# Performance work log

Measured on AMD Instinct MI355X. Metric: run time of the kernel, lower is better.

The kernel has to match this reference:

```python
import jax, jax.numpy as jnp
import numpy as np

DIM = 1024
HEADS = 8
HD = DIM // HEADS          # 128
HALF = HD // 2             # 64 complex pairs
EPS = 1e-6
T, L, H, W = 10, 4, 21, 37
TOK_PER_FRAME = 1 + L * (5 + H * W)   # 3129
SK = T * TOK_PER_FRAME                # 31290
SQ = 512
THETA = 10000.0


def _inv_freqs(dim):
    # matches precompute_freqs_cis: 1/theta**(arange(0,dim,2)/dim)
    return 1.0 / THETA ** (np.arange(0, dim, 2)[: dim // 2].astype(np.float64) / dim)


def _angles(t_idx, h_idx, w_idx):
    # 3D RoPE split per precompute_freqs_cis_3d: f gets HD-2*(HD//3)=44 dims, h/w get HD//3=42 each
    hd3 = HD // 3
    inv_f = _inv_freqs(HD - 2 * hd3)  # 22 freqs
    inv_h = _inv_freqs(hd3)           # 21 freqs
    inv_w = _inv_freqs(hd3)           # 21 freqs
    ang = np.concatenate([
        t_idx[:, None] * inv_f[None, :],
        h_idx[:, None] * inv_h[None, :],
        w_idx[:, None] * inv_w[None, :],
    ], axis=-1)  # [S, 64]
    return ang


def _memory_positions():
    # per-frame layout from build_3d_freqs_unified: 1 pose token (h=w=0),
    # then per layer: 5 register tokens (h=w=0) + H*W grid tokens
    h_f, w_f = [0], [0]
    grid_h, grid_w = np.meshgrid(np.arange(H), np.arange(W), indexing='ij')
    for _ in range(L):
        h_f += [0] * 5 + list(grid_h.ravel())
        w_f += [0] * 5 + list(grid_w.ravel())
    h_f = np.asarray(h_f, np.float64)
    w_f = np.asarray(w_f, np.float64)
    t_idx = np.repeat(np.arange(T, dtype=np.float64), TOK_PER_FRAME)
    return t_idx, np.tile(h_f, T), np.tile(w_f, T)


def setup_inputs() -> dict:
    key = jax.random.key(0)
    ks = jax.random.split(key, 8)
    # RoPE angle tables
    tq = np.zeros(SQ)  # use_time_encoding=False for queries -> t=0
    hq = (np.arange(SQ) // W) % H
    wq = np.arange(SQ) % W
    ang_q = _angles(tq.astype(np.float64), hq.astype(np.float64), wq.astype(np.float64))
    tk, hk, wk = _memory_positions()
    ang_k = _angles(tk, hk, wk)
    s = 0.02
    inp = {
        'x': jax.random.normal(ks[0], (1, SQ, DIM), jnp.float32),
        'mem': jax.random.normal(ks[1], (1, SK, DIM), jnp.float32),
        'mask': jax.random.randint(ks[2], (1, SK), 0, 2) > 0,
        'cos_q': jnp.asarray(np.cos(ang_q), jnp.float32),
        'sin_q': jnp.asarray(np.sin(ang_q), jnp.float32),
        'cos_k': jnp.asarray(np.cos(ang_k), jnp.float32),
        'sin_k': jnp.asarray(np.sin(ang_k), jnp.float32),
        'Wq': jax.random.normal(ks[3], (DIM, DIM), jnp.float32) * s,
        'bq': jnp.zeros((DIM,), jnp.float32),
        'Wk': jax.random.normal(ks[4], (DIM, DIM), jnp.float32) * s,
        'bk': jnp.zeros((DIM,), jnp.float32),
        'Wv': jax.random.normal(ks[5], (DIM, DIM), jnp.float32) * s,
        'bv': jnp.zeros((DIM,), jnp.float32),
        'Wo': jax.random.normal(ks[6], (DIM, DIM), jnp.float32) * s,
        'bo': jnp.zeros((DIM,), jnp.float32),
        'gq': jnp.ones((DIM,), jnp.float32),
        'gk': jnp.ones((DIM,), jnp.float32),
    }
    return inp


def _rmsnorm(x, g):
    xf = x.astype(jnp.float32)
    y = xf * jax.lax.rsqrt(jnp.mean(xf * xf, axis=-1, keepdims=True) + EPS)
    return y.astype(x.dtype) * g


def _rope(x, cos, sin):
    # x: [B,S,D]; complex rotation on interleaved pairs per head, freqs shared across heads
    B, S, _ = x.shape
    xh = x.reshape(B, S, HEADS, HALF, 2)
    xr, xi = xh[..., 0], xh[..., 1]
    c = cos[None, :, None, :]
    s = sin[None, :, None, :]
    orr = xr * c - xi * s
    oi = xr * s + xi * c
    return jnp.stack([orr, oi], axis=-1).reshape(B, S, HEADS * HD)


def reference(x, mem, mask, cos_q, sin_q, cos_k, sin_k,
              Wq, bq, Wk, bk, Wv, bv, Wo, bo, gq, gk):
    q = _rmsnorm(x @ Wq.T + bq, gq)
    k = _rmsnorm(mem @ Wk.T + bk, gk)
    v = mem @ Wv.T + bv
    q = _rope(q, cos_q, sin_q)
    k = _rope(k, cos_k, sin_k)
    B, Sq, _ = q.shape
    Sk = k.shape[1]
    qh = q.reshape(B, Sq, HEADS, HD)
    kh = k.reshape(B, Sk, HEADS, HD)
    vh = v.reshape(B, Sk, HEADS, HD)
    scores = jnp.einsum('bqnd,bknd->bnqk', qh, kh) / jnp.sqrt(jnp.float32(HD))
    bias = jnp.where(mask[:, None, None, :], 0.0, -jnp.inf).astype(scores.dtype)
    attn = jax.nn.softmax(scores + bias, axis=-1)
    out = jnp.einsum('bnqk,bknd->bqnd', attn, vh).reshape(B, Sq, DIM)
    return out @ Wo.T + bo
```

## Files before the change

### kernel.cpp

```cpp
#include <hip/hip_runtime.h>
#include <cstdint>

typedef __bf16 bf16;
typedef __bf16 bf16x8 __attribute__((ext_vector_type(8)));
typedef __bf16 bf16x4 __attribute__((ext_vector_type(4)));
typedef float f32x4 __attribute__((ext_vector_type(4)));

#define DEVINL __device__ __forceinline__

namespace {
constexpr int DIM = 1024, HEADS = 8, HD = 128, HALF = 64;
constexpr int SQ = 512;
constexpr int SK = 31290;
constexpr int SKP = 31488;
constexpr int NSPLIT = 24;
constexpr int NCHUNK = 31;

constexpr long OFF_MEMB = 0;
constexpr long OFF_XB   = OFF_MEMB + (long)SKP * DIM * 2;
constexpr long OFF_WKV  = OFF_XB + (long)SQ * DIM * 2;
constexpr long OFF_WQ   = OFF_WKV + 2048L * DIM * 2;
constexpr long OFF_WO   = OFF_WQ + (long)DIM * DIM * 2;
constexpr long OFF_BKV  = OFF_WO + (long)DIM * DIM * 2;
constexpr long OFF_KPRE = OFF_BKV + 2048L * 4;
constexpr long OFF_VT   = OFF_KPRE + (long)SKP * DIM * 2;
constexpr long OFF_QPRE = OFF_VT + (long)DIM * SKP * 2;
constexpr long OFF_QR   = OFF_QPRE + (long)SQ * DIM * 4;
constexpr long OFF_ML   = OFF_QR + (long)SQ * DIM * 2;
constexpr long OFF_AO   = OFF_ML + (long)NSPLIT * HEADS * SQ * 2 * 4;
constexpr long OFF_IDX  = OFF_AO + (long)SQ * DIM * 2;
constexpr long OFF_NKC  = OFF_IDX + 31744L * 4;
constexpr long OFF_CSM  = OFF_NKC + 64;
constexpr long OFF_CBS  = OFF_CSM + 256;
constexpr long OFF_OP   = OFF_MEMB;
}

DEVINL void gl_lds16(const void* g, void* l) {
  __builtin_amdgcn_global_load_lds(
      (__attribute__((address_space(1))) void*)(void*)g,
      (__attribute__((address_space(3))) void*)l, 16, 0, 0);
}


__global__ __launch_bounds__(1024) void k_scan1(const int* __restrict__ mask,
                                                int* __restrict__ csum) {
  int tid = threadIdx.x, lane = tid & 63, wv = tid >> 6;
  __shared__ int wsum[16];
  long i = (long)blockIdx.x * 1024 + tid;
  int m = (i < SK) ? (mask[i] != 0) : 0;
  unsigned long long bal = __ballot(m);
  if (lane == 0) wsum[wv] = (int)__popcll(bal);
  __syncthreads();
  if (tid == 0) {
    int tot = 0;
    #pragma unroll
    for (int j = 0; j < 16; ++j) tot += wsum[j];
    csum[blockIdx.x] = tot;
  }
}

__global__ __launch_bounds__(64) void k_scan2(const int* __restrict__ csum,
                                              int* __restrict__ cbase,
                                              int* __restrict__ nkcp) {
  int lane = threadIdx.x;
  int v = (lane < NCHUNK) ? csum[lane] : 0;
  int p = v;
  #pragma unroll
  for (int off = 1; off < 64; off <<= 1) {
    int t = __shfl_up(p, off);
    if (lane >= off) p += t;
  }
  if (lane < NCHUNK) cbase[lane] = p - v;
  if (lane == NCHUNK - 1) *nkcp = p;
}

__global__ __launch_bounds__(1024) void k_scan3(const int* __restrict__ mask,
                                                const int* __restrict__ cbase,
                                                int* __restrict__ idx) {
  int tid = threadIdx.x, lane = tid & 63, wv = tid >> 6;
  __shared__ int wsum[16];
  long i = (long)blockIdx.x * 1024 + tid;
  int m = (i < SK) ? (mask[i] != 0) : 0;
  unsigned long long bal = __ballot(m);
  int wpre = (int)__popcll(bal & ((1ull << lane) - 1ull));
  if (lane == 0) wsum[wv] = (int)__popcll(bal);
  __syncthreads();
  int woff = 0;
  #pragma unroll
  for (int j = 0; j < 16; ++j) woff += (j < wv) ? wsum[j] : 0;
  if (m) idx[cbase[blockIdx.x] + woff + wpre] = (int)i;
}


__global__ __launch_bounds__(256) void k_cvt_mem(const float* __restrict__ mem,
                                                 const int* __restrict__ idx,
                                                 const int* __restrict__ nkcp,
                                                 bf16* __restrict__ memb) {
  long i = (long)blockIdx.x * 256 + threadIdx.x;
  long e = i * 8;
  if (e >= (long)SKP * DIM) return;
  int row = (int)(e >> 10);
  int nkc = *nkcp;
  int lim = ((((nkc + 63) & ~63) + 255) & ~255);
  if (row >= lim) return;
  bf16x8 o;
  if (row < nkc) {
    long se = ((long)idx[row] << 10) + (e & 1023);
    float4 a = *(const float4*)(mem + se);
    float4 b = *(const float4*)(mem + se + 4);
    o[0] = (bf16)a.x; o[1] = (bf16)a.y; o[2] = (bf16)a.z; o[3] = (bf16)a.w;
    o[4] = (bf16)b.x; o[5] = (bf16)b.y; o[6] = (bf16)b.z; o[7] = (bf16)b.w;
  } else {
    #pragma unroll
    for (int j = 0; j < 8; ++j) o[j] = (bf16)0.0f;
  }
  *(bf16x8*)(memb + e) = o;
}

__global__ __launch_bounds__(256) void k_prep(const float* __restrict__ x,
    const float* __restrict__ Wq, const float* __restrict__ Wo,
    const float* __restrict__ Wk, const float* __restrict__ Wv,
    const float* __restrict__ bk, const float* __restrict__ bv,
    bf16* __restrict__ xb, bf16* __restrict__ WqB, bf16* __restrict__ WoB,
    bf16* __restrict__ WkvB, float* __restrict__ bKV) {
  long i = (long)blockIdx.x * 256 + threadIdx.x;
  constexpr long n_x = 65536, n_w = 131072;
  const float* src;
  bf16* dst;
  long off;
  if (i < n_x) { src = x; dst = xb; off = i; }
  else if (i < n_x + n_w) { src = Wq; dst = WqB; off = i - n_x; }
  else if (i < n_x + 2 * n_w) { src = Wo; dst = WoB; off = i - n_x - n_w; }
  else if (i < n_x + 2 * n_w + 262144) {
    long j = i - n_x - 2 * n_w;
    long e = j * 8;
    int n = (int)(e >> 10);
    const float* s2 = (n < 1024) ? (Wk + e) : (Wv + e - 1024L * 1024);
    float4 a = *(const float4*)(s2);
    float4 b = *(const float4*)(s2 + 4);
    bf16x8 o;
    o[0] = (bf16)a.x; o[1] = (bf16)a.y; o[2] = (bf16)a.z; o[3] = (bf16)a.w;
    o[4] = (bf16)b.x; o[5] = (bf16)b.y; o[6] = (bf16)b.z; o[7] = (bf16)b.w;
    *(bf16x8*)(WkvB + e) = o;
    if (j < 2048) bKV[j] = (j < 1024) ? bk[j] : bv[j - 1024];
    return;
  } else return;
  long e = off * 8;
  float4 a = *(const float4*)(src + e);
  float4 b = *(const float4*)(src + e + 4);
  bf16x8 o;
  o[0] = (bf16)a.x; o[1] = (bf16)a.y; o[2] = (bf16)a.z; o[3] = (bf16)a.w;
  o[4] = (bf16)b.x; o[5] = (bf16)b.y; o[6] = (bf16)b.z; o[7] = (bf16)b.w;
  *(bf16x8*)(dst + e) = o;
}


template<int MODE>
__global__ __launch_bounds__(256, 2)
void k_gemm(const bf16* __restrict__ A, const bf16* __restrict__ B,
            const float* __restrict__ bias, int Mtiles, int Ntiles,
            float* __restrict__ outF, int ldF,
            bf16* __restrict__ outK, bf16* __restrict__ outVT) {
  constexpr int K = 1024;
  __shared__ char lds[32768];
  char* ldsA = lds;
  char* ldsB = lds + 16384;
  int tid = threadIdx.x;
  int w = tid >> 6, lane = tid & 63;
  int cpx = gridDim.x >> 3;
  int bid = (blockIdx.x & 7) * cpx + (blockIdx.x >> 3);
  int mt = bid / Ntiles, nt = bid % Ntiles;
  int m0 = mt * 128, n0 = nt * 128;
  int wm = w >> 1, wn = w & 1;
  int cl = lane & 15, rg = lane >> 4;

  f32x4 acc[4][4] = {};

  int rowi = lane >> 3, g = lane & 7;
  for (int kt = 0; kt < K / 64; ++kt) {
    #pragma unroll
    for (int j = 0; j < 4; ++j) {
      int rb = (w * 4 + j) * 8;
      int row = rb + rowi;
      int gs = g ^ (row & 7);
      gl_lds16((const char*)(A + (long)(m0 + row) * K + kt * 64) + gs * 16, ldsA + rb * 128);
      gl_lds16((const char*)(B + (long)(n0 + row) * K + kt * 64) + gs * 16, ldsB + rb * 128);
    }
    __syncthreads();
    #pragma unroll
    for (int ks = 0; ks < 2; ++ks) {
      bf16x8 af[4], bfr[4];
      #pragma unroll
      for (int i = 0; i < 4; ++i) {
        int rowA = wm * 64 + i * 16 + cl;
        int c = ks * 4 + rg;
        af[i] = *(const bf16x8*)(ldsA + rowA * 128 + ((c ^ (rowA & 7)) * 16));
        int rowB = wn * 64 + i * 16 + cl;
        bfr[i] = *(const bf16x8*)(ldsB + rowB * 128 + ((c ^ (rowB & 7)) * 16));
      }
      #pragma unroll
      for (int mf = 0; mf < 4; ++mf)
        #pragma unroll
        for (int nf = 0; nf < 4; ++nf)
          acc[mf][nf] = __builtin_amdgcn_mfma_f32_16x16x32_bf16(af[mf], bfr[nf], acc[mf][nf], 0, 0, 0);
    }
    __syncthreads();
  }

  #pragma unroll
  for (int mf = 0; mf < 4; ++mf) {
    #pragma unroll
    for (int nf = 0; nf < 4; ++nf) {
      int n = n0 + wn * 64 + nf * 16 + cl;
      float bval = bias[n];
      int mb = m0 + wm * 64 + mf * 16 + rg * 4;
      #pragma unroll
      for (int rr = 0; rr < 4; ++rr)
        outF[(long)(mb + rr) * ldF + n] = acc[mf][nf][rr] + bval;
    }
  }
}


#define KV_PHASE(P)                                                                   \
  {                                                                                   \
    bf16x8 a00 = dsA(cur, 2 * (P), 0),     a01 = dsA(cur, 2 * (P), 1);                \
    bf16x8 a10 = dsA(cur, 2 * (P) + 1, 0), a11 = dsA(cur, 2 * (P) + 1, 1);            \
    __builtin_amdgcn_s_setprio(1);                                                    \
    _Pragma("unroll")                                                                 \
    for (int nf = 0; nf < 4; ++nf) {                                                  \
      acc[2 * (P)][nf]     = __builtin_amdgcn_mfma_f32_16x16x32_bf16(a00, bb[nf][0], acc[2 * (P)][nf], 0, 0, 0);     \
      acc[2 * (P) + 1][nf] = __builtin_amdgcn_mfma_f32_16x16x32_bf16(a10, bb[nf][0], acc[2 * (P) + 1][nf], 0, 0, 0); \
    }                                                                                 \
    _Pragma("unroll")                                                                 \
    for (int nf = 0; nf < 4; ++nf) {                                                  \
      acc[2 * (P)][nf]     = __builtin_amdgcn_mfma_f32_16x16x32_bf16(a01, bb[nf][1], acc[2 * (P)][nf], 0, 0, 0);     \
      acc[2 * (P) + 1][nf] = __builtin_amdgcn_mfma_f32_16x16x32_bf16(a11, bb[nf][1], acc[2 * (P) + 1][nf], 0, 0, 0); \
    }                                                                                 \
    __builtin_amdgcn_s_setprio(0);                                                    \
  }

__global__ __launch_bounds__(512)
void k_gemm_kv(const bf16* __restrict__ A, const bf16* __restrict__ B,
               const float* __restrict__ bias, const int* __restrict__ nkcp,
               bf16* __restrict__ outK, bf16* __restrict__ outVT) {
  constexpr int K = 1024, NTK = 16;
  __shared__ char lds[131072];
  const int tid = threadIdx.x;
  const int w = tid >> 6, lane = tid & 63;
  const int mt = blockIdx.x >> 3, nt = blockIdx.x & 7;
  const int m0 = mt * 256, n0 = nt * 256;
  if (m0 >= ((*nkcp + 63) & ~63)) return;
  const int wm = w >> 2, wn = w & 3;
  const int cl = lane & 15, rg = lane >> 4;
  const int srow = lane >> 3, sg = lane & 7;

  f32x4 acc[8][4] = {};

  auto stage = [&](int b, int kt, int isB, int cr) {
    const bf16* src = isB ? B : A;
    int r = cr + w * 8 + srow;
    int gs = sg ^ (r & 7);
    const char* gp = (const char*)(src + (long)((isB ? n0 : m0) + r) * K + kt * 64) + gs * 16;
    char* lp = lds + b * 65536 + isB * 32768 + (cr + w * 8) * 128;
    gl_lds16(gp, lp);
  };
  auto dsA = [&](int b, int mf, int ks) -> bf16x8 {
    int r = wm * 128 + mf * 16 + cl;
    int c = ks * 4 + rg;
    return *(const bf16x8*)(lds + b * 65536 + r * 128 + ((c ^ (r & 7)) * 16));
  };
  auto dsB = [&](int b, int nf, int ks) -> bf16x8 {
    int r = wn * 64 + nf * 16 + cl;
    int c = ks * 4 + rg;
    return *(const bf16x8*)(lds + b * 65536 + 32768 + r * 128 + ((c ^ (r & 7)) * 16));
  };

  stage(0, 0, 1, 0);   stage(0, 0, 1, 64);
  stage(0, 0, 1, 128); stage(0, 0, 1, 192);
  stage(0, 0, 0, 0);   stage(0, 0, 0, 128);
  stage(0, 0, 0, 64);  stage(0, 0, 0, 192);

  for (int t = 0; t < NTK; ++t) {
    const int cur = t & 1, nxt = cur ^ 1;
    const bool pre = (t + 1 < NTK);
    bf16x8 bb[4][2];

    if (pre) {
      stage(nxt, t + 1, 1, 0); stage(nxt, t + 1, 1, 64);
      asm volatile("s_waitcnt vmcnt(4)\ns_barrier" ::: "memory");
    } else {
      asm volatile("s_waitcnt vmcnt(2)\ns_barrier" ::: "memory");
    }
    #pragma unroll
    for (int nf = 0; nf < 4; ++nf) { bb[nf][0] = dsB(cur, nf, 0); bb[nf][1] = dsB(cur, nf, 1); }
    KV_PHASE(0)
    asm volatile("s_barrier" ::: "memory");
    if (pre) {
      stage(nxt, t + 1, 1, 128); stage(nxt, t + 1, 1, 192);
      stage(nxt, t + 1, 0, 0);   stage(nxt, t + 1, 0, 128);
    }
    KV_PHASE(1)
    asm volatile("s_barrier" ::: "memory");
    if (pre) {
      stage(nxt, t + 1, 0, 64); stage(nxt, t + 1, 0, 192);
      asm volatile("s_waitcnt vmcnt(8)\ns_barrier" ::: "memory");
    } else {
      asm volatile("s_waitcnt vmcnt(0)\ns_barrier" ::: "memory");
    }
    KV_PHASE(2)
    asm volatile("s_barrier" ::: "memory");
    KV_PHASE(3)
    asm volatile("s_barrier" ::: "memory");
  }

  if (nt < 4) {
    #pragma unroll
    for (int mf = 0; mf < 8; ++mf)
      #pragma unroll
      for (int nf = 0; nf < 4; ++nf) {
        int n = n0 + wn * 64 + nf * 16 + cl;
        float bval = bias[n];
        int mrow = m0 + wm * 128 + mf * 16 + rg * 4;
        #pragma unroll
        for (int rr = 0; rr < 4; ++rr)
          outK[(long)(mrow + rr) * 1024 + n] = (bf16)(acc[mf][nf][rr] + bval);
      }
  } else {
    #pragma unroll
    for (int mf = 0; mf < 8; ++mf)
      #pragma unroll
      for (int nf = 0; nf < 4; ++nf) {
        int n = n0 + wn * 64 + nf * 16 + cl;
        float bval = bias[n];
        int mrow = m0 + wm * 128 + mf * 16 + rg * 4;
        bf16x4 pk;
        #pragma unroll
        for (int rr = 0; rr < 4; ++rr) pk[rr] = (bf16)(acc[mf][nf][rr] + bval);
        *(bf16x4*)(outVT + (long)(n - 1024) * SKP + mrow) = pk;
      }
  }
}


__global__ __launch_bounds__(256) void k_fuse_q(const float* __restrict__ QP,
    bf16* __restrict__ Qr, const float* __restrict__ gg,
    const float* __restrict__ cosT, const float* __restrict__ sinT) {
  int row = blockIdx.x, tid = threadIdx.x;
  int d0 = tid * 4;
  float4 t = *(const float4*)(QP + (long)row * DIM + d0);
  float v0 = t.x, v1 = t.y, v2 = t.z, v3 = t.w;
  float ss = v0 * v0 + v1 * v1 + v2 * v2 + v3 * v3;
  #pragma unroll
  for (int m = 1; m < 64; m <<= 1) ss += __shfl_xor(ss, m);
  __shared__ float red[4];
  if ((tid & 63) == 0) red[tid >> 6] = ss;
  __syncthreads();
  float rn = rsqrtf((red[0] + red[1] + red[2] + red[3]) * (1.0f / DIM) + 1e-6f);
  v0 *= rn * gg[d0]; v1 *= rn * gg[d0 + 1]; v2 *= rn * gg[d0 + 2]; v3 *= rn * gg[d0 + 3];
  int i0 = (d0 & 127) >> 1;
  float c0 = cosT[(long)row * HALF + i0], s0 = sinT[(long)row * HALF + i0];
  float c1 = cosT[(long)row * HALF + i0 + 1], s1 = sinT[(long)row * HALF + i0 + 1];
  bf16x4 o = { (bf16)(v0 * c0 - v1 * s0), (bf16)(v0 * s0 + v1 * c0),
               (bf16)(v2 * c1 - v3 * s1), (bf16)(v2 * s1 + v3 * c1) };
  *(bf16x4*)(Qr + (long)row * DIM + d0) = o;
}

__global__ __launch_bounds__(256) void k_fuse_k(bf16* __restrict__ KP,
    const float* __restrict__ gg, const float* __restrict__ cosT,
    const float* __restrict__ sinT, const int* __restrict__ idx,
    const int* __restrict__ nkcp) {
  int row = blockIdx.x, tid = threadIdx.x;
  int nkc = *nkcp;
  if (row >= ((nkc + 63) & ~63)) return;
  int orig = (row < nkc) ? idx[row] : 0;
  int d0 = tid * 4;
  bf16x4 t = *(const bf16x4*)(KP + (long)row * DIM + d0);
  float v0 = (float)t[0], v1 = (float)t[1], v2 = (float)t[2], v3 = (float)t[3];
  float ss = v0 * v0 + v1 * v1 + v2 * v2 + v3 * v3;
  #pragma unroll
  for (int m = 1; m < 64; m <<= 1) ss += __shfl_xor(ss, m);
  __shared__ float red[4];
  if ((tid & 63) == 0) red[tid >> 6] = ss;
  __syncthreads();
  float rn = rsqrtf((red[0] + red[1] + red[2] + red[3]) * (1.0f / DIM) + 1e-6f);
  v0 *= rn * gg[d0]; v1 *= rn * gg[d0 + 1]; v2 *= rn * gg[d0 + 2]; v3 *= rn * gg[d0 + 3];
  int i0 = (d0 & 127) >> 1;
  float c0 = cosT[(long)orig * HALF + i0], s0 = sinT[(long)orig * HALF + i0];
  float c1 = cosT[(long)orig * HALF + i0 + 1], s1 = sinT[(long)orig * HALF + i0 + 1];
  bf16x4 o = { (bf16)(v0 * c0 - v1 * s0), (bf16)(v0 * s0 + v1 * c0),
               (bf16)(v2 * c1 - v3 * s1), (bf16)(v2 * s1 + v3 * c1) };
  *(bf16x4*)(KP + (long)row * DIM + d0) = o;
}


__global__ __launch_bounds__(256, 2)
void k_attn(const bf16* __restrict__ Kr, const bf16* __restrict__ VT,
            const bf16* __restrict__ Qr, const int* __restrict__ nkcp,
            float* __restrict__ Opart, float* __restrict__ ml) {
  __shared__ char lds[51200];
  char* ldsK = lds;
  char* ldsV = lds + 16384;
  int tid = threadIdx.x, w = tid >> 6, lane = tid & 63;
  char* ldsP = lds + 32768 + w * 4608;
  int bid = blockIdx.x;
  int swz = (bid & 7) * 96 + (bid >> 3);
  int sp = swz >> 5, h = (swz >> 2) & 7, qb = swz & 3;
  int nkc = *nkcp;
  int NTC = (nkc + 63) >> 6;
  int t0 = (sp * NTC) / NSPLIT;
  int t1 = ((sp + 1) * NTC) / NSPLIT;
  int cl = lane & 15, rg = lane >> 4;
  int qbase = qb * 128 + w * 32;

  bf16x8 qf[2][4];
  #pragma unroll
  for (int mf = 0; mf < 2; ++mf)
    #pragma unroll
    for (int ks = 0; ks < 4; ++ks)
      qf[mf][ks] = *(const bf16x8*)(Qr + (long)(qbase + mf * 16 + cl) * DIM + h * HD + ks * 32 + rg * 8);

  f32x4 Oa[2][8] = {};
  float m_r[2] = {-1e30f, -1e30f};
  float l_r[2] = {0.f, 0.f};

  const float sc = 0.08838834764831845f;
  for (int t = t0; t < t1; ++t) {
    int k0 = t * 64;
    __syncthreads();
    {
      int rK = lane >> 4, gK = lane & 15;
      #pragma unroll
      for (int j = 0; j < 4; ++j) {
        int rb = w * 16 + j * 4;
        int row = rb + rK;
        int gs = gK ^ (row & 7);
        gl_lds16((const char*)(Kr + (long)(k0 + row) * DIM + h * HD) + gs * 16,
                 ldsK + rb * 256);
      }
      int rV = lane >> 3, gV = lane & 7;
      #pragma unroll
      for (int j = 0; j < 4; ++j) {
        int db = w * 32 + j * 8;
        int d = db + rV;
        int gs = gV ^ (d & 7);
        gl_lds16((const char*)(VT + (long)(h * HD + d) * SKP + k0) + gs * 16,
                 ldsV + db * 128);
      }
    }
    __syncthreads();

    f32x4 sa[2][4] = {};
    #pragma unroll
    for (int ks = 0; ks < 4; ++ks) {
      #pragma unroll
      for (int nf = 0; nf < 4; ++nf) {
        int key = nf * 16 + cl;
        int c = ks * 4 + rg;
        bf16x8 kb = *(const bf16x8*)(ldsK + key * 256 + ((c ^ (key & 7)) * 16));
        sa[0][nf] = __builtin_amdgcn_mfma_f32_16x16x32_bf16(kb, qf[0][ks], sa[0][nf], 0, 0, 0);
        sa[1][nf] = __builtin_amdgcn_mfma_f32_16x16x32_bf16(kb, qf[1][ks], sa[1][nf], 0, 0, 0);
      }
    }

    #pragma unroll
    for (int mf = 0; mf < 2; ++mf) {
      #pragma unroll
      for (int nf = 0; nf < 4; ++nf)
        #pragma unroll
        for (int r = 0; r < 4; ++r) {
          int key = k0 + nf * 16 + rg * 4 + r;
          sa[mf][nf][r] = (key < nkc) ? sa[mf][nf][r] * sc : -1e30f;
        }
      float mx = sa[mf][0][0];
      #pragma unroll
      for (int nf = 0; nf < 4; ++nf)
        #pragma unroll
        for (int r = 0; r < 4; ++r) mx = fmaxf(mx, sa[mf][nf][r]);
      mx = fmaxf(mx, __shfl_xor(mx, 16));
      mx = fmaxf(mx, __shfl_xor(mx, 32));
      bool grew = mx > m_r[mf] + 6.0f;
      if (__any(grew)) {
        float mn = grew ? mx : m_r[mf];
        float scl = __expf(m_r[mf] - mn);
        m_r[mf] = mn;
        l_r[mf] *= scl;
        int sb = lane & 48;
        float s0 = __shfl(scl, sb | (rg * 4 + 0));
        float s1 = __shfl(scl, sb | (rg * 4 + 1));
        float s2 = __shfl(scl, sb | (rg * 4 + 2));
        float s3 = __shfl(scl, sb | (rg * 4 + 3));
        #pragma unroll
        for (int df = 0; df < 8; ++df) {
          Oa[mf][df][0] *= s0; Oa[mf][df][1] *= s1;
          Oa[mf][df][2] *= s2; Oa[mf][df][3] *= s3;
        }
      }
      float rsum = 0.f;
      #pragma unroll
      for (int nf = 0; nf < 4; ++nf)
        #pragma unroll
        for (int r = 0; r < 4; ++r) {
          float p = __expf(sa[mf][nf][r] - m_r[mf]);
          sa[mf][nf][r] = p;
          rsum += p;
        }
      rsum += __shfl_xor(rsum, 16);
      rsum += __shfl_xor(rsum, 32);
      l_r[mf] += rsum;
      char* prow = ldsP + (mf * 16 + cl) * 144;
      #pragma unroll
      for (int nf = 0; nf < 4; ++nf) {
        bf16x4 pk = { (bf16)sa[mf][nf][0], (bf16)sa[mf][nf][1],
                      (bf16)sa[mf][nf][2], (bf16)sa[mf][nf][3] };
        *(bf16x4*)(prow + nf * 32 + rg * 8) = pk;
      }
    }

    #pragma unroll
    for (int ks = 0; ks < 2; ++ks) {
      bf16x8 pa0 = *(const bf16x8*)(ldsP + cl * 144 + ks * 64 + rg * 16);
      bf16x8 pa1 = *(const bf16x8*)(ldsP + (16 + cl) * 144 + ks * 64 + rg * 16);
      int c = ks * 4 + rg;
      #pragma unroll
      for (int df = 0; df < 8; ++df) {
        int d = df * 16 + cl;
        bf16x8 vb = *(const bf16x8*)(ldsV + d * 128 + ((c ^ (d & 7)) * 16));
        Oa[0][df] = __builtin_amdgcn_mfma_f32_16x16x32_bf16(pa0, vb, Oa[0][df], 0, 0, 0);
        Oa[1][df] = __builtin_amdgcn_mfma_f32_16x16x32_bf16(pa1, vb, Oa[1][df], 0, 0, 0);
      }
    }
  }

  long rowb = (long)(sp * HEADS + h) * SQ + qbase;
  #pragma unroll
  for (int mf = 0; mf < 2; ++mf) {
    #pragma unroll
    for (int df = 0; df < 8; ++df)
      #pragma unroll
      for (int r = 0; r < 4; ++r) {
        int qr = mf * 16 + rg * 4 + r;
        Opart[(rowb + qr) * HD + df * 16 + cl] = Oa[mf][df][r];
      }
  }
  if (rg == 0) {
    #pragma unroll
    for (int mf = 0; mf < 2; ++mf) {
      ml[(rowb + mf * 16 + cl) * 2] = m_r[mf];
      ml[(rowb + mf * 16 + cl) * 2 + 1] = l_r[mf];
    }
  }
}

__global__ __launch_bounds__(128) void k_combine(const float* __restrict__ Opart,
    const float* __restrict__ ml, bf16* __restrict__ AO) {
  int bid = blockIdx.x;
  int h = bid >> 9, qq = bid & 511;
  int d = threadIdx.x;
  float M = -1e30f;
  #pragma unroll 4
  for (int s2 = 0; s2 < NSPLIT; ++s2) {
    long mi = (long)(s2 * HEADS + h) * SQ + qq;
    M = fmaxf(M, ml[mi * 2]);
  }
  float L = 0.f, acc = 0.f;
  #pragma unroll 4
  for (int s2 = 0; s2 < NSPLIT; ++s2) {
    long mi = (long)(s2 * HEADS + h) * SQ + qq;
    float wgt = __expf(ml[mi * 2] - M);
    L += wgt * ml[mi * 2 + 1];
    acc += wgt * Opart[mi * HD + d];
  }
  AO[(long)qq * DIM + h * HD + d] = (bf16)(acc / L);
}


extern "C" void kernel_launch(void* const* d_in, const int* in_sizes, int n_in,
                              void* d_out, int out_size, void* d_ws, size_t ws_size,
                              hipStream_t stream) {
  const float* x     = (const float*)d_in[0];
  const float* mem   = (const float*)d_in[1];
  const int*   mask  = (const int*)d_in[2];
  const float* cos_q = (const float*)d_in[3];
  const float* sin_q = (const float*)d_in[4];
  const float* cos_k = (const float*)d_in[5];
  const float* sin_k = (const float*)d_in[6];
  const float* Wq    = (const float*)d_in[7];
  const float* bq    = (const float*)d_in[8];
  const float* Wk    = (const float*)d_in[9];
  const float* bk    = (const float*)d_in[10];
  const float* Wv    = (const float*)d_in[11];
  const float* bv    = (const float*)d_in[12];
  const float* Wo    = (const float*)d_in[13];
  const float* bo    = (const float*)d_in[14];
  const float* gq    = (const float*)d_in[15];
  const float* gk    = (const float*)d_in[16];

  char* ws = (char*)d_ws;
  bf16*  memb = (bf16*)(ws + OFF_MEMB);
  bf16*  xb   = (bf16*)(ws + OFF_XB);
  bf16*  WkvB = (bf16*)(ws + OFF_WKV);
  bf16*  WqB  = (bf16*)(ws + OFF_WQ);
  bf16*  WoB  = (bf16*)(ws + OFF_WO);
  float* bKV  = (float*)(ws + OFF_BKV);
  bf16*  Kpre = (bf16*)(ws + OFF_KPRE);
  bf16*  VT   = (bf16*)(ws + OFF_VT);
  float* Qpre = (float*)(ws + OFF_QPRE);
  bf16*  Qr   = (bf16*)(ws + OFF_QR);
  float* Opart= (float*)(ws + OFF_OP);
  float* mlb  = (float*)(ws + OFF_ML);
  bf16*  AO   = (bf16*)(ws + OFF_AO);
  int*   idx  = (int*)(ws + OFF_IDX);
  int*   nkcp = (int*)(ws + OFF_NKC);
  int*   csum = (int*)(ws + OFF_CSM);
  int*   cbase= (int*)(ws + OFF_CBS);

  k_scan1<<<dim3(NCHUNK), dim3(1024), 0, stream>>>(mask, csum);
  k_scan2<<<dim3(1), dim3(64), 0, stream>>>(csum, cbase, nkcp);
  k_scan3<<<dim3(NCHUNK), dim3(1024), 0, stream>>>(mask, cbase, idx);
  k_cvt_mem<<<dim3(SKP * DIM / 8 / 256), dim3(256), 0, stream>>>(mem, idx, nkcp, memb);
  k_prep<<<dim3(2304), dim3(256), 0, stream>>>(x, Wq, Wo, Wk, Wv, bk, bv,
                                               xb, WqB, WoB, WkvB, bKV);

  k_gemm<0><<<dim3(4 * 8), dim3(256), 0, stream>>>(xb, WqB, bq, 4, 8, Qpre, DIM,
                                                   (bf16*)nullptr, (bf16*)nullptr);
  k_gemm_kv<<<dim3(984), dim3(512), 0, stream>>>(memb, WkvB, bKV, nkcp, Kpre, VT);

  k_fuse_q<<<dim3(SQ), dim3(256), 0, stream>>>(Qpre, Qr, gq, cos_q, sin_q);
  k_fuse_k<<<dim3(SKP), dim3(256), 0, stream>>>(Kpre, gk, cos_k, sin_k, idx, nkcp);

  k_attn<<<dim3(NSPLIT * HEADS * 4), dim3(256), 0, stream>>>(Kpre, VT, Qr, nkcp, Opart, mlb);
  k_combine<<<dim3(HEADS * SQ), dim3(128), 0, stream>>>(Opart, mlb, AO);

  k_gemm<0><<<dim3(4 * 8), dim3(256), 0, stream>>>(AO, WoB, bo, 4, 8, (float*)d_out, DIM,
                                                   (bf16*)nullptr, (bf16*)nullptr);
  (void)in_sizes; (void)n_in; (void)out_size; (void)ws_size;
}
```

Measured before the change: 236.7 us.

## Fuse scan kernels, trim GEMM barriers, split attention waits, store partials in bf16

Folds the single-block prefix scan into the index-scatter kernel so each block sums the chunk counts itself, removing one launch. Drops intermediate barriers in the KV GEMM main loop and replaces a full sync in attention with partial vmcnt waits, to reduce stall time. Attention partial outputs are written as bf16 instead of fp32, halving the combine traffic at some precision cost. Removing barriers risks LDS read/write hazards if the staging schedule does not guarantee separation.

```diff
diff --git a/kernel.cpp b/kernel.cpp
--- a/kernel.cpp
+++ b/kernel.cpp
@@ -31,7 +31,6 @@
 constexpr long OFF_IDX  = OFF_AO + (long)SQ * DIM * 2;
 constexpr long OFF_NKC  = OFF_IDX + 31744L * 4;
 constexpr long OFF_CSM  = OFF_NKC + 64;
-constexpr long OFF_CBS  = OFF_CSM + 256;
 constexpr long OFF_OP   = OFF_MEMB;
 }
 
@@ -59,26 +58,20 @@
   }
 }
 
-__global__ __launch_bounds__(64) void k_scan2(const int* __restrict__ csum,
-                                              int* __restrict__ cbase,
-                                              int* __restrict__ nkcp) {
-  int lane = threadIdx.x;
-  int v = (lane < NCHUNK) ? csum[lane] : 0;
-  int p = v;
-  #pragma unroll
-  for (int off = 1; off < 64; off <<= 1) {
-    int t = __shfl_up(p, off);
-    if (lane >= off) p += t;
-  }
-  if (lane < NCHUNK) cbase[lane] = p - v;
-  if (lane == NCHUNK - 1) *nkcp = p;
-}
-
 __global__ __launch_bounds__(1024) void k_scan3(const int* __restrict__ mask,
-                                                const int* __restrict__ cbase,
-                                                int* __restrict__ idx) {
+                                                const int* __restrict__ csum,
+                                                int* __restrict__ idx,
+                                                int* __restrict__ nkcp) {
   int tid = threadIdx.x, lane = tid & 63, wv = tid >> 6;
   __shared__ int wsum[16];
+  int cb = 0, tot = 0;
+  #pragma unroll
+  for (int j = 0; j < NCHUNK; ++j) {
+    int v = csum[j];
+    if (j < (int)blockIdx.x) cb += v;
+    tot += v;
+  }
+  if (blockIdx.x == 0 && tid == 0) *nkcp = tot;
   long i = (long)blockIdx.x * 1024 + tid;
   int m = (i < SK) ? (mask[i] != 0) : 0;
   unsigned long long bal = __ballot(m);
@@ -88,7 +81,7 @@
   int woff = 0;
   #pragma unroll
   for (int j = 0; j < 16; ++j) woff += (j < wv) ? wsum[j] : 0;
-  if (m) idx[cbase[blockIdx.x] + woff + wpre] = (int)i;
+  if (m) idx[cb + woff + wpre] = (int)i;
 }
 
 
@@ -295,13 +288,11 @@
     #pragma unroll
     for (int nf = 0; nf < 4; ++nf) { bb[nf][0] = dsB(cur, nf, 0); bb[nf][1] = dsB(cur, nf, 1); }
     KV_PHASE(0)
-    asm volatile("s_barrier" ::: "memory");
     if (pre) {
       stage(nxt, t + 1, 1, 128); stage(nxt, t + 1, 1, 192);
       stage(nxt, t + 1, 0, 0);   stage(nxt, t + 1, 0, 128);
     }
     KV_PHASE(1)
-    asm volatile("s_barrier" ::: "memory");
     if (pre) {
       stage(nxt, t + 1, 0, 64); stage(nxt, t + 1, 0, 192);
       asm volatile("s_waitcnt vmcnt(8)\ns_barrier" ::: "memory");
@@ -309,7 +300,6 @@
       asm volatile("s_waitcnt vmcnt(0)\ns_barrier" ::: "memory");
     }
     KV_PHASE(2)
-    asm volatile("s_barrier" ::: "memory");
     KV_PHASE(3)
     asm volatile("s_barrier" ::: "memory");
   }
@@ -397,7 +387,7 @@
 __global__ __launch_bounds__(256, 2)
 void k_attn(const bf16* __restrict__ Kr, const bf16* __restrict__ VT,
             const bf16* __restrict__ Qr, const int* __restrict__ nkcp,
-            float* __restrict__ Opart, float* __restrict__ ml) {
+            bf16* __restrict__ Opart, float* __restrict__ ml) {
   __shared__ char lds[51200];
   char* ldsK = lds;
   char* ldsV = lds + 16384;
@@ -448,7 +438,7 @@
                  ldsV + db * 128);
       }
     }
-    __syncthreads();
+    asm volatile("s_waitcnt vmcnt(4)\ns_barrier" ::: "memory");
 
     f32x4 sa[2][4] = {};
     #pragma unroll
@@ -517,6 +507,8 @@
       }
     }
 
+    asm volatile("s_waitcnt vmcnt(0)\ns_barrier" ::: "memory");
+
     #pragma unroll
     for (int ks = 0; ks < 2; ++ks) {
       bf16x8 pa0 = *(const bf16x8*)(ldsP + cl * 144 + ks * 64 + rg * 16);
@@ -540,7 +532,7 @@
       #pragma unroll
       for (int r = 0; r < 4; ++r) {
         int qr = mf * 16 + rg * 4 + r;
-        Opart[(rowb + qr) * HD + df * 16 + cl] = Oa[mf][df][r];
+        Opart[(rowb + qr) * HD + df * 16 + cl] = (bf16)Oa[mf][df][r];
       }
   }
   if (rg == 0) {
@@ -552,7 +544,7 @@
   }
 }
 
-__global__ __launch_bounds__(128) void k_combine(const float* __restrict__ Opart,
+__global__ __launch_bounds__(128) void k_combine(const bf16* __restrict__ Opart,
     const float* __restrict__ ml, bf16* __restrict__ AO) {
   int bid = blockIdx.x;
   int h = bid >> 9, qq = bid & 511;
@@ -569,7 +561,7 @@
     long mi = (long)(s2 * HEADS + h) * SQ + qq;
     float wgt = __expf(ml[mi * 2] - M);
     L += wgt * ml[mi * 2 + 1];
-    acc += wgt * Opart[mi * HD + d];
+    acc += wgt * (float)Opart[mi * HD + d];
   }
   AO[(long)qq * DIM + h * HD + d] = (bf16)(acc / L);
 }
@@ -607,17 +599,15 @@
   bf16*  VT   = (bf16*)(ws + OFF_VT);
   float* Qpre = (float*)(ws + OFF_QPRE);
   bf16*  Qr   = (bf16*)(ws + OFF_QR);
-  float* Opart= (float*)(ws + OFF_OP);
+  bf16*  Opart= (bf16*)(ws + OFF_OP);
   float* mlb  = (float*)(ws + OFF_ML);
   bf16*  AO   = (bf16*)(ws + OFF_AO);
   int*   idx  = (int*)(ws + OFF_IDX);
   int*   nkcp = (int*)(ws + OFF_NKC);
   int*   csum = (int*)(ws + OFF_CSM);
-  int*   cbase= (int*)(ws + OFF_CBS);
 
   k_scan1<<<dim3(NCHUNK), dim3(1024), 0, stream>>>(mask, csum);
-  k_scan2<<<dim3(1), dim3(64), 0, stream>>>(csum, cbase, nkcp);
-  k_scan3<<<dim3(NCHUNK), dim3(1024), 0, stream>>>(mask, cbase, idx);
+  k_scan3<<<dim3(NCHUNK), dim3(1024), 0, stream>>>(mask, csum, idx, nkcp);
   k_cvt_mem<<<dim3(SKP * DIM / 8 / 256), dim3(256), 0, stream>>>(mem, idx, nkcp, memb);
   k_prep<<<dim3(2304), dim3(256), 0, stream>>>(x, Wq, Wo, Wk, Wv, bk, bv,
                                                xb, WqB, WoB, WkvB, bKV);
```

New measurement: 227.8 us. 3.7% less time.
